# Kernel optimization log

Hardware: AMD Instinct MI355X
Metric: run time of the kernel (lower is better)

## Reference

```python
import jax, jax.numpy as jnp
import numpy as np

E, T, D, N_RBF, N_SBF = 262144, 1048576, 128, 6, 42


def setup_inputs() -> dict:
    key = jax.random.key(0)
    ks = jax.random.split(key, 24)
    s = 0.05
    inp = {
        "m_ji": jax.random.normal(ks[0], (E, D), jnp.float32),
        "e_rbf": jax.random.normal(ks[1], (E, N_RBF), jnp.float32),
        "a_sbf": jax.random.normal(ks[2], (T, N_SBF), jnp.float32),
        "nbr_list": jax.random.randint(ks[3], (E, 2), 0, 65536),
        "kj_idx": jax.random.randint(ks[4], (T,), 0, E),
        "ji_idx": jax.random.randint(ks[5], (T,), 0, E),
        # edge branch params
        "We": jax.random.normal(ks[6], (N_RBF, D), jnp.float32) * s,
        "W_e1": jax.random.normal(ks[7], (D, D), jnp.float32) * s,
        "b_e1": jnp.zeros((D,), jnp.float32),
        "W_e2": jax.random.normal(ks[8], (D, D), jnp.float32) * s,
        "b_e2": jnp.zeros((D,), jnp.float32),
        "W_e3": jax.random.normal(ks[9], (D, D), jnp.float32) * s,
        "b_e3": jnp.zeros((D,), jnp.float32),
        "W_e4": jax.random.normal(ks[10], (D, D), jnp.float32) * s,
        # angle branch params
        "Wa": jax.random.normal(ks[11], (N_SBF, D), jnp.float32) * s,
        "W_a1": jax.random.normal(ks[12], (D, D), jnp.float32) * s,
        "b_a1": jnp.zeros((D,), jnp.float32),
        "W_a2": jax.random.normal(ks[13], (D, D), jnp.float32) * s,
        "b_a2": jnp.zeros((D,), jnp.float32),
        "W_a3": jax.random.normal(ks[14], (D, D), jnp.float32) * s,
        "b_a3": jnp.zeros((D,), jnp.float32),
        "W_a4": jax.random.normal(ks[15], (D, D), jnp.float32) * s,
    }
    return inp


def _mlp(x, W1, b1, W2, b2, W3, b3, W4):
    x = jax.nn.silu(x @ W1 + b1)
    x = jax.nn.silu(x @ W2 + b2)
    x = jax.nn.silu(x @ W3 + b3)
    return x @ W4


def reference(m_ji, e_rbf, a_sbf, nbr_list, kj_idx, ji_idx,
              We, W_e1, b_e1, W_e2, b_e2, W_e3, b_e3, W_e4,
              Wa, W_a1, b_a1, W_a2, b_a2, W_a3, b_a3, W_a4):
    # edge branch: project rbf to embed dim, gate by edge messages  [E, D]
    edge_feats = _mlp((e_rbf @ We) * m_ji, W_e1, b_e1, W_e2, b_e2, W_e3, b_e3, W_e4)
    # angle branch: project sbf, gate by triplet-gathered message sum  [T, D]
    angle_gate = m_ji[kj_idx] + m_ji[ji_idx]
    angle_feats = _mlp((a_sbf @ Wa) * angle_gate, W_a1, b_a1, W_a2, b_a2, W_a3, b_a3, W_a4)
    return (edge_feats, angle_feats)
```

## Files before the change

### kernel.cpp

```cpp
#include <hip/hip_runtime.h>
#include <stdint.h>

typedef __attribute__((ext_vector_type(8))) short bf16x8;
typedef __attribute__((ext_vector_type(4))) float f32x4;
typedef __attribute__((ext_vector_type(8))) unsigned short us8;

static __device__ __forceinline__ unsigned short f2bf_u(float f) {
  __bf16 h = (__bf16)f;
  return __builtin_bit_cast(unsigned short, h);
}
static __device__ __forceinline__ uint32_t pack2bf(float a, float b) {
  return (uint32_t)f2bf_u(a) | ((uint32_t)f2bf_u(b) << 16);
}
static __device__ __forceinline__ float silu_f(float v) {
  float e = __builtin_amdgcn_exp2f(v * -1.44269504088896341f);
  return v * __builtin_amdgcn_rcpf(1.0f + e);
}

template<bool LAST>
static __device__ __forceinline__ void xlayer(
    const char* __restrict__ src, char* __restrict__ dst,
    const bf16x8* wf, const float* __restrict__ bias,
    float* __restrict__ gout, int l15, int q, int w, int rs)
{
  f32x4 bv;
  if (!LAST) bv = *(const f32x4*)(bias + w * 16 + q * 4);
  #pragma unroll
  for (int rg = 0; rg < 8; ++rg) {
    const int row = rg * 16 + l15;
    f32x4 acc = {0.f, 0.f, 0.f, 0.f};
    #pragma unroll
    for (int ks = 0; ks < 4; ++ks) {
      bf16x8 xf = *(const bf16x8*)(src + ((row * 256 + ks * 64 + q * 16) ^ rs));
      acc = __builtin_amdgcn_mfma_f32_16x16x32_bf16(wf[ks], xf, acc, 0, 0, 0);
    }
    if (!LAST) {
      float v0 = silu_f(acc[0] + bv[0]);
      float v1 = silu_f(acc[1] + bv[1]);
      float v2 = silu_f(acc[2] + bv[2]);
      float v3 = silu_f(acc[3] + bv[3]);
      uint2 u; u.x = pack2bf(v0, v1); u.y = pack2bf(v2, v3);
      *(uint2*)(dst + ((row * 256 + w * 32 + q * 8) ^ rs)) = u;
    } else {
      __builtin_nontemporal_store(acc,
          (f32x4*)(gout + (size_t)row * 128 + w * 16 + q * 4));
    }
  }
}

__global__ __launch_bounds__(512)
__attribute__((amdgpu_waves_per_eu(4, 4)))
void angle_kernel(
    const float* __restrict__ m_ji, const float* __restrict__ a_sbf,
    const int* __restrict__ kj, const int* __restrict__ ji,
    const float* __restrict__ b1, const float* __restrict__ b2,
    const float* __restrict__ b3,
    const char* __restrict__ wt4, const char* __restrict__ waT,
    float* __restrict__ out)
{
  extern __shared__ char lds[];
  char* xbA = lds;
  char* xbB = lds + 32768;
  char* aux = lds + 65536;
  const int tid = threadIdx.x, lane = tid & 63, w = tid >> 6;
  const int l15 = lane & 15, q = lane >> 4;
  const int rs = (l15 & 7) << 4;
  const size_t tb = (size_t)blockIdx.x * 128;

  bf16x8 wa0 = *(const bf16x8*)(waT + (w * 2 + 0) * 1024 + lane * 16);
  bf16x8 wa1 = *(const bf16x8*)(waT + (w * 2 + 1) * 1024 + lane * 16);

  int ikj[8], iji[8];
  #pragma unroll
  for (int g = 0; g < 8; ++g) {
    ikj[g] = kj[tb + g * 16 + l15];
    iji[g] = ji[tb + g * 16 + l15];
  }

  f32x4 pk[8], pj[8];
  #pragma unroll
  for (int g = 0; g < 8; ++g) {
    pk[g] = *(const f32x4*)(m_ji + (size_t)ikj[g] * 128 + w * 16 + q * 4);
    pj[g] = *(const f32x4*)(m_ji + (size_t)iji[g] * 128 + w * 16 + q * 4);
  }
  __builtin_amdgcn_sched_barrier(0);

  {
    const float* src = a_sbf + tb * 42;
    #pragma unroll
    for (int j2 = 0; j2 < 8; ++j2) {
      const int i = tid + j2 * 512;
      const int row = i >> 5, p = i & 31;
      const float* rp = src + row * 42 + p * 2;
      float v0 = (p * 2 < 42) ? __builtin_nontemporal_load(rp) : 0.f;
      float v1 = (p * 2 + 1 < 42) ? __builtin_nontemporal_load(rp + 1) : 0.f;
      *(uint32_t*)(aux + ((row * 128 + p * 4) ^ ((row & 7) << 4))) = pack2bf(v0, v1);
    }
  }
  __syncthreads();

  #pragma unroll
  for (int rg = 0; rg < 8; ++rg) {
    const int row = rg * 16 + l15;
    bf16x8 x0f = *(const bf16x8*)(aux + ((row * 128 + q * 16) ^ rs));
    bf16x8 x1f = *(const bf16x8*)(aux + ((row * 128 + 64 + q * 16) ^ rs));
    f32x4 acc = {0.f, 0.f, 0.f, 0.f};
    acc = __builtin_amdgcn_mfma_f32_16x16x32_bf16(wa0, x0f, acc, 0, 0, 0);
    acc = __builtin_amdgcn_mfma_f32_16x16x32_bf16(wa1, x1f, acc, 0, 0, 0);
    f32x4 g = pk[rg] + pj[rg];
    uint2 u;
    u.x = pack2bf(acc[0] * g[0], acc[1] * g[1]);
    u.y = pack2bf(acc[2] * g[2], acc[3] * g[3]);
    *(uint2*)(xbA + ((row * 256 + w * 32 + q * 8) ^ rs)) = u;
  }
  __builtin_amdgcn_sched_barrier(0);

  bf16x8 wfl[4][4];
  #pragma unroll
  for (int L = 0; L < 4; ++L)
    #pragma unroll
    for (int ks = 0; ks < 4; ++ks)
      wfl[L][ks] = *(const bf16x8*)(wt4 + L * 32768 + (w * 4 + ks) * 1024 + lane * 16);

  __syncthreads();

  xlayer<false>(xbA, xbB, wfl[0], b1, nullptr, l15, q, w, rs);
  __syncthreads();
  xlayer<false>(xbB, xbA, wfl[1], b2, nullptr, l15, q, w, rs);
  __syncthreads();
  xlayer<false>(xbA, xbB, wfl[2], b3, nullptr, l15, q, w, rs);
  __syncthreads();
  xlayer<true>(xbB, nullptr, wfl[3], nullptr, out + tb * 128, l15, q, w, rs);
}

__global__ __launch_bounds__(512)
__attribute__((amdgpu_waves_per_eu(4, 4)))
void edge_kernel(
    const float* __restrict__ m_ji, const float* __restrict__ e_rbf,
    const float* __restrict__ b1, const float* __restrict__ b2,
    const float* __restrict__ b3,
    const char* __restrict__ wt4, const char* __restrict__ weT,
    float* __restrict__ out)
{
  extern __shared__ char lds[];
  char* xbA = lds;
  char* xbB = lds + 32768;
  float* auxF = (float*)(lds + 65536);
  const int tid = threadIdx.x, lane = tid & 63, w = tid >> 6;
  const int l15 = lane & 15, q = lane >> 4;
  const int rs = (l15 & 7) << 4;
  const size_t tb = (size_t)blockIdx.x * 128;

  bf16x8 we = *(const bf16x8*)(weT + w * 1024 + lane * 16);

  f32x4 mr[8];
  #pragma unroll
  for (int g = 0; g < 8; ++g)
    mr[g] = *(const f32x4*)(m_ji + (tb + g * 16 + l15) * 128 + w * 16 + q * 4);
  __builtin_amdgcn_sched_barrier(0);

  {
    const float* src = e_rbf + tb * 6;
    auxF[tid] = __builtin_nontemporal_load(src + tid);
    const int i2 = tid + 512;
    if (i2 < 768) auxF[i2] = __builtin_nontemporal_load(src + i2);
  }
  __syncthreads();

  #pragma unroll
  for (int rg = 0; rg < 8; ++rg) {
    const int row = rg * 16 + l15;
    bf16x8 ef;
    #pragma unroll
    for (int j = 0; j < 8; ++j) {
      float v = (j < 6) ? auxF[row * 6 + j] : 0.f;
      unsigned short h = (q == 0 && j < 6) ? f2bf_u(v) : (unsigned short)0;
      ef[j] = (short)h;
    }
    f32x4 acc = {0.f, 0.f, 0.f, 0.f};
    acc = __builtin_amdgcn_mfma_f32_16x16x32_bf16(we, ef, acc, 0, 0, 0);
    f32x4 g = mr[rg];
    uint2 u;
    u.x = pack2bf(acc[0] * g[0], acc[1] * g[1]);
    u.y = pack2bf(acc[2] * g[2], acc[3] * g[3]);
    *(uint2*)(xbA + ((row * 256 + w * 32 + q * 8) ^ rs)) = u;
  }
  __builtin_amdgcn_sched_barrier(0);

  bf16x8 wfl[4][4];
  #pragma unroll
  for (int L = 0; L < 4; ++L)
    #pragma unroll
    for (int ks = 0; ks < 4; ++ks)
      wfl[L][ks] = *(const bf16x8*)(wt4 + L * 32768 + (w * 4 + ks) * 1024 + lane * 16);

  __syncthreads();

  xlayer<false>(xbA, xbB, wfl[0], b1, nullptr, l15, q, w, rs);
  __syncthreads();
  xlayer<false>(xbB, xbA, wfl[1], b2, nullptr, l15, q, w, rs);
  __syncthreads();
  xlayer<false>(xbA, xbB, wfl[2], b3, nullptr, l15, q, w, rs);
  __syncthreads();
  xlayer<true>(xbB, nullptr, wfl[3], nullptr, out + tb * 128, l15, q, w, rs);
}

__global__ void prep_kernel(
    const float* __restrict__ W0, const float* __restrict__ W1,
    const float* __restrict__ W2, const float* __restrict__ W3,
    const float* __restrict__ W4, const float* __restrict__ W5,
    const float* __restrict__ W6, const float* __restrict__ W7,
    const float* __restrict__ Wa, const float* __restrict__ We,
    char* __restrict__ ws)
{
  const int gid = blockIdx.x * 256 + threadIdx.x;
  const int lane = gid & 63;
  const int l15 = lane & 15, q = lane >> 4;
  if (gid < 16384) {
    const int mat = gid >> 11;
    const int ctks = (gid & 2047) >> 6;
    const int n = (ctks >> 2) * 16 + l15;
    const int k0 = (ctks & 3) * 32 + q * 8;
    const float* W;
    switch (mat) {
      case 0: W = W0; break; case 1: W = W1; break;
      case 2: W = W2; break; case 3: W = W3; break;
      case 4: W = W4; break; case 5: W = W5; break;
      case 6: W = W6; break; default: W = W7; break;
    }
    us8 v;
    #pragma unroll
    for (int j = 0; j < 8; ++j) v[j] = f2bf_u(W[(size_t)(k0 + j) * 128 + n]);
    *(us8*)(ws + mat * 32768 + ctks * 1024 + lane * 16) = v;
  } else if (gid < 17408) {
    const int g = gid - 16384;
    const int ctks = g >> 6;
    const int n = (ctks >> 1) * 16 + l15;
    const int k0 = (ctks & 1) * 32 + q * 8;
    us8 v;
    #pragma unroll
    for (int j = 0; j < 8; ++j) {
      const int k = k0 + j;
      v[j] = (k < 42) ? f2bf_u(Wa[(size_t)k * 128 + n]) : (unsigned short)0;
    }
    *(us8*)(ws + 262144 + ctks * 1024 + lane * 16) = v;
  } else if (gid < 17920) {
    const int g = gid - 17408;
    const int ct = g >> 6;
    const int n = ct * 16 + l15;
    const int k0 = q * 8;
    us8 v;
    #pragma unroll
    for (int j = 0; j < 8; ++j) {
      const int k = k0 + j;
      v[j] = (k < 6) ? f2bf_u(We[(size_t)k * 128 + n]) : (unsigned short)0;
    }
    *(us8*)(ws + 278528 + ct * 1024 + lane * 16) = v;
  }
}

extern "C" void kernel_launch(void* const* d_in, const int* in_sizes, int n_in,
                              void* d_out, int out_size, void* d_ws, size_t ws_size,
                              hipStream_t stream) {
  (void)in_sizes; (void)n_in; (void)out_size; (void)ws_size;
  const float* m_ji  = (const float*)d_in[0];
  const float* e_rbf = (const float*)d_in[1];
  const float* a_sbf = (const float*)d_in[2];
  const int*   kj    = (const int*)d_in[4];
  const int*   ji    = (const int*)d_in[5];
  const float* We    = (const float*)d_in[6];
  const float* We1   = (const float*)d_in[7];
  const float* be1   = (const float*)d_in[8];
  const float* We2   = (const float*)d_in[9];
  const float* be2   = (const float*)d_in[10];
  const float* We3   = (const float*)d_in[11];
  const float* be3   = (const float*)d_in[12];
  const float* We4   = (const float*)d_in[13];
  const float* Wa    = (const float*)d_in[14];
  const float* Wa1   = (const float*)d_in[15];
  const float* ba1   = (const float*)d_in[16];
  const float* Wa2   = (const float*)d_in[17];
  const float* ba2   = (const float*)d_in[18];
  const float* Wa3   = (const float*)d_in[19];
  const float* ba3   = (const float*)d_in[20];
  const float* Wa4   = (const float*)d_in[21];
  char* ws = (char*)d_ws;
  float* out = (float*)d_out;

  hipFuncSetAttribute((const void*)edge_kernel,
                      hipFuncAttributeMaxDynamicSharedMemorySize, 68608);
  hipFuncSetAttribute((const void*)angle_kernel,
                      hipFuncAttributeMaxDynamicSharedMemorySize, 81920);

  prep_kernel<<<70, 256, 0, stream>>>(
      We1, We2, We3, We4, Wa1, Wa2, Wa3, Wa4, Wa, We, ws);
  edge_kernel<<<262144 / 128, 512, 68608, stream>>>(
      m_ji, e_rbf, be1, be2, be3, ws, ws + 278528, out);
  angle_kernel<<<1048576 / 128, 512, 81920, stream>>>(
      m_ji, a_sbf, kj, ji, ba1, ba2, ba3, ws + 131072, ws + 262144,
      out + (size_t)262144 * 128);
}
```

Measured before the change: 615.7 us.

## Shrink MLP blocks to 32 rows with two waves and stream weights per layer

Both the edge and angle kernels now use 128-thread blocks that each handle 32 rows. Each wave computes four 16-column tiles across two row groups. The input projections load a_sbf and e_rbf rows straight from global memory into MFMA fragments, dropping the LDS staging pass. LDS use falls to 16 KB per block, and layer weights are reloaded from global or cache inside each layer instead of being held in registers. The aim is higher occupancy and less per-block setup and synchronisation, at the cost of several times more weight traffic through the caches per row processed.

```diff
diff --git a/kernel.cpp b/kernel.cpp
--- a/kernel.cpp
+++ b/kernel.cpp
@@ -4,52 +4,81 @@
 typedef __attribute__((ext_vector_type(8))) short bf16x8;
 typedef __attribute__((ext_vector_type(4))) float f32x4;
 typedef __attribute__((ext_vector_type(8))) unsigned short us8;
+typedef __bf16 bf16v2 __attribute__((ext_vector_type(2)));
+
+#define T_CNT 1048576
+#define E_CNT 262144
 
 static __device__ __forceinline__ unsigned short f2bf_u(float f) {
   __bf16 h = (__bf16)f;
   return __builtin_bit_cast(unsigned short, h);
 }
 static __device__ __forceinline__ uint32_t pack2bf(float a, float b) {
-  return (uint32_t)f2bf_u(a) | ((uint32_t)f2bf_u(b) << 16);
+  bf16v2 t; t[0] = (__bf16)a; t[1] = (__bf16)b;
+  return __builtin_bit_cast(uint32_t, t);
 }
 static __device__ __forceinline__ float silu_f(float v) {
   float e = __builtin_amdgcn_exp2f(v * -1.44269504088896341f);
   return v * __builtin_amdgcn_rcpf(1.0f + e);
 }
+static __device__ __forceinline__ bf16x8 frag8(f32x4 a, f32x4 b) {
+  union { bf16x8 v; uint32_t u[4]; } r;
+  r.u[0] = pack2bf(a[0], a[1]); r.u[1] = pack2bf(a[2], a[3]);
+  r.u[2] = pack2bf(b[0], b[1]); r.u[3] = pack2bf(b[2], b[3]);
+  return r.v;
+}
 
 template<bool LAST>
-static __device__ __forceinline__ void xlayer(
+static __device__ __forceinline__ void layer_mfma(
     const char* __restrict__ src, char* __restrict__ dst,
-    const bf16x8* wf, const float* __restrict__ bias,
-    float* __restrict__ gout, int l15, int q, int w, int rs)
-{
-  f32x4 bv;
-  if (!LAST) bv = *(const f32x4*)(bias + w * 16 + q * 4);
-  #pragma unroll
-  for (int rg = 0; rg < 8; ++rg) {
+    const char* __restrict__ wbase,
+    const float* __restrict__ bias,
+    float* __restrict__ gout,
+    int l15, int q, int w, int rs)
+{
+  f32x4 acc[2][4];
+  #pragma unroll
+  for (int rg = 0; rg < 2; ++rg)
+    #pragma unroll
+    for (int c = 0; c < 4; ++c) { f32x4 z = {0.f,0.f,0.f,0.f}; acc[rg][c] = z; }
+
+  const int lane16 = (l15 | (q << 4)) * 16;
+  #pragma unroll
+  for (int ks = 0; ks < 4; ++ks) {
+    bf16x8 wf[4];
+    #pragma unroll
+    for (int c = 0; c < 4; ++c)
+      wf[c] = *(const bf16x8*)(wbase + (((w * 4 + c) * 4 + ks) << 10) + lane16);
+    bf16x8 xf0 = *(const bf16x8*)(src + ((l15 * 256 + ks * 64 + q * 16) ^ rs));
+    bf16x8 xf1 = *(const bf16x8*)(src + (((16 + l15) * 256 + ks * 64 + q * 16) ^ rs));
+    #pragma unroll
+    for (int c = 0; c < 4; ++c) {
+      acc[0][c] = __builtin_amdgcn_mfma_f32_16x16x32_bf16(wf[c], xf0, acc[0][c], 0, 0, 0);
+      acc[1][c] = __builtin_amdgcn_mfma_f32_16x16x32_bf16(wf[c], xf1, acc[1][c], 0, 0, 0);
+    }
+  }
+
+  #pragma unroll
+  for (int rg = 0; rg < 2; ++rg) {
     const int row = rg * 16 + l15;
-    f32x4 acc = {0.f, 0.f, 0.f, 0.f};
-    #pragma unroll
-    for (int ks = 0; ks < 4; ++ks) {
-      bf16x8 xf = *(const bf16x8*)(src + ((row * 256 + ks * 64 + q * 16) ^ rs));
-      acc = __builtin_amdgcn_mfma_f32_16x16x32_bf16(wf[ks], xf, acc, 0, 0, 0);
-    }
-    if (!LAST) {
-      float v0 = silu_f(acc[0] + bv[0]);
-      float v1 = silu_f(acc[1] + bv[1]);
-      float v2 = silu_f(acc[2] + bv[2]);
-      float v3 = silu_f(acc[3] + bv[3]);
-      uint2 u; u.x = pack2bf(v0, v1); u.y = pack2bf(v2, v3);
-      *(uint2*)(dst + ((row * 256 + w * 32 + q * 8) ^ rs)) = u;
-    } else {
-      __builtin_nontemporal_store(acc,
-          (f32x4*)(gout + (size_t)row * 128 + w * 16 + q * 4));
-    }
-  }
-}
-
-__global__ __launch_bounds__(512)
-__attribute__((amdgpu_waves_per_eu(4, 4)))
+    #pragma unroll
+    for (int c = 0; c < 4; ++c) {
+      if (!LAST) {
+        f32x4 bv = *(const f32x4*)(bias + w * 64 + c * 16 + q * 4);
+        uint2 u;
+        u.x = pack2bf(silu_f(acc[rg][c][0] + bv[0]), silu_f(acc[rg][c][1] + bv[1]));
+        u.y = pack2bf(silu_f(acc[rg][c][2] + bv[2]), silu_f(acc[rg][c][3] + bv[3]));
+        *(uint2*)(dst + ((row * 256 + w * 128 + c * 32 + q * 8) ^ rs)) = u;
+      } else {
+        __builtin_nontemporal_store(acc[rg][c],
+            (f32x4*)(gout + (size_t)row * 128 + w * 64 + c * 16 + q * 4));
+      }
+    }
+  }
+}
+
+__global__ __launch_bounds__(128)
+__attribute__((amdgpu_waves_per_eu(4, 5)))
 void angle_kernel(
     const float* __restrict__ m_ji, const float* __restrict__ a_sbf,
     const int* __restrict__ kj, const int* __restrict__ ji,
@@ -58,83 +87,60 @@
     const char* __restrict__ wt4, const char* __restrict__ waT,
     float* __restrict__ out)
 {
-  extern __shared__ char lds[];
-  char* xbA = lds;
-  char* xbB = lds + 32768;
-  char* aux = lds + 65536;
+  __shared__ __align__(16) char xbA[8192];
+  __shared__ __align__(16) char xbB[8192];
   const int tid = threadIdx.x, lane = tid & 63, w = tid >> 6;
   const int l15 = lane & 15, q = lane >> 4;
   const int rs = (l15 & 7) << 4;
-  const size_t tb = (size_t)blockIdx.x * 128;
-
-  bf16x8 wa0 = *(const bf16x8*)(waT + (w * 2 + 0) * 1024 + lane * 16);
-  bf16x8 wa1 = *(const bf16x8*)(waT + (w * 2 + 1) * 1024 + lane * 16);
-
-  int ikj[8], iji[8];
-  #pragma unroll
-  for (int g = 0; g < 8; ++g) {
-    ikj[g] = kj[tb + g * 16 + l15];
-    iji[g] = ji[tb + g * 16 + l15];
-  }
-
-  f32x4 pk[8], pj[8];
-  #pragma unroll
-  for (int g = 0; g < 8; ++g) {
-    pk[g] = *(const f32x4*)(m_ji + (size_t)ikj[g] * 128 + w * 16 + q * 4);
-    pj[g] = *(const f32x4*)(m_ji + (size_t)iji[g] * 128 + w * 16 + q * 4);
-  }
-  __builtin_amdgcn_sched_barrier(0);
-
-  {
-    const float* src = a_sbf + tb * 42;
-    #pragma unroll
-    for (int j2 = 0; j2 < 8; ++j2) {
-      const int i = tid + j2 * 512;
-      const int row = i >> 5, p = i & 31;
-      const float* rp = src + row * 42 + p * 2;
-      float v0 = (p * 2 < 42) ? __builtin_nontemporal_load(rp) : 0.f;
-      float v1 = (p * 2 + 1 < 42) ? __builtin_nontemporal_load(rp + 1) : 0.f;
-      *(uint32_t*)(aux + ((row * 128 + p * 4) ^ ((row & 7) << 4))) = pack2bf(v0, v1);
-    }
-  }
-  __syncthreads();
-
-  #pragma unroll
-  for (int rg = 0; rg < 8; ++rg) {
+  const size_t tb = (size_t)blockIdx.x * 32;
+  const int lane16 = lane * 16;
+
+  #pragma unroll
+  for (int rg = 0; rg < 2; ++rg) {
     const int row = rg * 16 + l15;
-    bf16x8 x0f = *(const bf16x8*)(aux + ((row * 128 + q * 16) ^ rs));
-    bf16x8 x1f = *(const bf16x8*)(aux + ((row * 128 + 64 + q * 16) ^ rs));
-    f32x4 acc = {0.f, 0.f, 0.f, 0.f};
-    acc = __builtin_amdgcn_mfma_f32_16x16x32_bf16(wa0, x0f, acc, 0, 0, 0);
-    acc = __builtin_amdgcn_mfma_f32_16x16x32_bf16(wa1, x1f, acc, 0, 0, 0);
-    f32x4 g = pk[rg] + pj[rg];
-    uint2 u;
-    u.x = pack2bf(acc[0] * g[0], acc[1] * g[1]);
-    u.y = pack2bf(acc[2] * g[2], acc[3] * g[3]);
-    *(uint2*)(xbA + ((row * 256 + w * 32 + q * 8) ^ rs)) = u;
-  }
-  __builtin_amdgcn_sched_barrier(0);
-
-  bf16x8 wfl[4][4];
-  #pragma unroll
-  for (int L = 0; L < 4; ++L)
-    #pragma unroll
-    for (int ks = 0; ks < 4; ++ks)
-      wfl[L][ks] = *(const bf16x8*)(wt4 + L * 32768 + (w * 4 + ks) * 1024 + lane * 16);
-
-  __syncthreads();
-
-  xlayer<false>(xbA, xbB, wfl[0], b1, nullptr, l15, q, w, rs);
-  __syncthreads();
-  xlayer<false>(xbB, xbA, wfl[1], b2, nullptr, l15, q, w, rs);
-  __syncthreads();
-  xlayer<false>(xbA, xbB, wfl[2], b3, nullptr, l15, q, w, rs);
-  __syncthreads();
-  xlayer<true>(xbB, nullptr, wfl[3], nullptr, out + tb * 128, l15, q, w, rs);
-}
-
-__global__ __launch_bounds__(512)
-__attribute__((amdgpu_waves_per_eu(4, 4)))
+    const size_t grow = tb + row;
+    const int ikj = kj[grow], iji = ji[grow];
+    const float* ap = a_sbf + grow * 42;
+    f32x4 a0 = *(const f32x4*)(ap + q * 8);
+    f32x4 a1 = *(const f32x4*)(ap + q * 8 + 4);
+    f32x4 c0 = {0.f,0.f,0.f,0.f}, c1 = {0.f,0.f,0.f,0.f};
+    if (q == 0) { c0 = *(const f32x4*)(ap + 32); c1 = *(const f32x4*)(ap + 36); }
+    else if (q == 1) { float2 t = *(const float2*)(ap + 40); c0[0] = t.x; c0[1] = t.y; }
+    bf16x8 f0 = frag8(a0, a1);
+    bf16x8 f1 = frag8(c0, c1);
+    #pragma unroll
+    for (int c = 0; c < 4; ++c) {
+      const int ct = w * 4 + c;
+      bf16x8 wa0 = *(const bf16x8*)(waT + ((ct * 2 + 0) << 10) + lane16);
+      bf16x8 wa1 = *(const bf16x8*)(waT + ((ct * 2 + 1) << 10) + lane16);
+      f32x4 acc = {0.f,0.f,0.f,0.f};
+      acc = __builtin_amdgcn_mfma_f32_16x16x32_bf16(wa0, f0, acc, 0, 0, 0);
+      acc = __builtin_amdgcn_mfma_f32_16x16x32_bf16(wa1, f1, acc, 0, 0, 0);
+      const float* bk = m_ji + (size_t)ikj * 128 + ct * 16 + q * 4;
+      const float* bj = m_ji + (size_t)iji * 128 + ct * 16 + q * 4;
+      f32x4 pk = *(const f32x4*)(bk);
+      f32x4 pj = *(const f32x4*)(bj);
+      f32x4 g = pk + pj;
+      uint2 u;
+      u.x = pack2bf(acc[0] * g[0], acc[1] * g[1]);
+      u.y = pack2bf(acc[2] * g[2], acc[3] * g[3]);
+      *(uint2*)(xbA + ((row * 256 + w * 128 + c * 32 + q * 8) ^ rs)) = u;
+    }
+  }
+  __syncthreads();
+
+  layer_mfma<false>(xbA, xbB, wt4,           b1, nullptr, l15, q, w, rs);
+  __syncthreads();
+  layer_mfma<false>(xbB, xbA, wt4 + 32768,   b2, nullptr, l15, q, w, rs);
+  __syncthreads();
+  layer_mfma<false>(xbA, xbB, wt4 + 65536,   b3, nullptr, l15, q, w, rs);
+  __syncthreads();
+  layer_mfma<true >(xbB, nullptr, wt4 + 98304, nullptr,
+                    out + tb * 128, l15, q, w, rs);
+}
+
+__global__ __launch_bounds__(128)
+__attribute__((amdgpu_waves_per_eu(4, 5)))
 void edge_kernel(
     const float* __restrict__ m_ji, const float* __restrict__ e_rbf,
     const float* __restrict__ b1, const float* __restrict__ b2,
@@ -142,67 +148,49 @@
     const char* __restrict__ wt4, const char* __restrict__ weT,
     float* __restrict__ out)
 {
-  extern __shared__ char lds[];
-  char* xbA = lds;
-  char* xbB = lds + 32768;
-  float* auxF = (float*)(lds + 65536);
+  __shared__ __align__(16) char xbA[8192];
+  __shared__ __align__(16) char xbB[8192];
   const int tid = threadIdx.x, lane = tid & 63, w = tid >> 6;
   const int l15 = lane & 15, q = lane >> 4;
   const int rs = (l15 & 7) << 4;
-  const size_t tb = (size_t)blockIdx.x * 128;
-
-  bf16x8 we = *(const bf16x8*)(weT + w * 1024 + lane * 16);
-
-  f32x4 mr[8];
-  #pragma unroll
-  for (int g = 0; g < 8; ++g)
-    mr[g] = *(const f32x4*)(m_ji + (tb + g * 16 + l15) * 128 + w * 16 + q * 4);
-  __builtin_amdgcn_sched_barrier(0);
-
-  {
-    const float* src = e_rbf + tb * 6;
-    auxF[tid] = __builtin_nontemporal_load(src + tid);
-    const int i2 = tid + 512;
-    if (i2 < 768) auxF[i2] = __builtin_nontemporal_load(src + i2);
-  }
-  __syncthreads();
-
-  #pragma unroll
-  for (int rg = 0; rg < 8; ++rg) {
+  const size_t tb = (size_t)blockIdx.x * 32;
+  const int lane16 = lane * 16;
+
+  #pragma unroll
+  for (int rg = 0; rg < 2; ++rg) {
     const int row = rg * 16 + l15;
-    bf16x8 ef;
-    #pragma unroll
-    for (int j = 0; j < 8; ++j) {
-      float v = (j < 6) ? auxF[row * 6 + j] : 0.f;
-      unsigned short h = (q == 0 && j < 6) ? f2bf_u(v) : (unsigned short)0;
-      ef[j] = (short)h;
-    }
-    f32x4 acc = {0.f, 0.f, 0.f, 0.f};
-    acc = __builtin_amdgcn_mfma_f32_16x16x32_bf16(we, ef, acc, 0, 0, 0);
-    f32x4 g = mr[rg];
-    uint2 u;
-    u.x = pack2bf(acc[0] * g[0], acc[1] * g[1]);
-    u.y = pack2bf(acc[2] * g[2], acc[3] * g[3]);
-    *(uint2*)(xbA + ((row * 256 + w * 32 + q * 8) ^ rs)) = u;
-  }
-  __builtin_amdgcn_sched_barrier(0);
-
-  bf16x8 wfl[4][4];
-  #pragma unroll
-  for (int L = 0; L < 4; ++L)
-    #pragma unroll
-    for (int ks = 0; ks < 4; ++ks)
-      wfl[L][ks] = *(const bf16x8*)(wt4 + L * 32768 + (w * 4 + ks) * 1024 + lane * 16);
-
-  __syncthreads();
-
-  xlayer<false>(xbA, xbB, wfl[0], b1, nullptr, l15, q, w, rs);
-  __syncthreads();
-  xlayer<false>(xbB, xbA, wfl[1], b2, nullptr, l15, q, w, rs);
-  __syncthreads();
-  xlayer<false>(xbA, xbB, wfl[2], b3, nullptr, l15, q, w, rs);
-  __syncthreads();
-  xlayer<true>(xbB, nullptr, wfl[3], nullptr, out + tb * 128, l15, q, w, rs);
+    const size_t grow = tb + row;
+    const float* ep = e_rbf + grow * 6;
+    f32x4 a0 = {0.f,0.f,0.f,0.f}, a1 = {0.f,0.f,0.f,0.f};
+    if (q == 0) {
+      a0 = *(const f32x4*)(ep);
+      float2 t = *(const float2*)(ep + 4);
+      a1[0] = t.x; a1[1] = t.y;
+    }
+    bf16x8 ef = frag8(a0, a1);
+    #pragma unroll
+    for (int c = 0; c < 4; ++c) {
+      const int ct = w * 4 + c;
+      bf16x8 we = *(const bf16x8*)(weT + (ct << 10) + lane16);
+      f32x4 acc = {0.f,0.f,0.f,0.f};
+      acc = __builtin_amdgcn_mfma_f32_16x16x32_bf16(we, ef, acc, 0, 0, 0);
+      f32x4 g = *(const f32x4*)(m_ji + grow * 128 + ct * 16 + q * 4);
+      uint2 u;
+      u.x = pack2bf(acc[0] * g[0], acc[1] * g[1]);
+      u.y = pack2bf(acc[2] * g[2], acc[3] * g[3]);
+      *(uint2*)(xbA + ((row * 256 + w * 128 + c * 32 + q * 8) ^ rs)) = u;
+    }
+  }
+  __syncthreads();
+
+  layer_mfma<false>(xbA, xbB, wt4,           b1, nullptr, l15, q, w, rs);
+  __syncthreads();
+  layer_mfma<false>(xbB, xbA, wt4 + 32768,   b2, nullptr, l15, q, w, rs);
+  __syncthreads();
+  layer_mfma<false>(xbA, xbB, wt4 + 65536,   b3, nullptr, l15, q, w, rs);
+  __syncthreads();
+  layer_mfma<true >(xbB, nullptr, wt4 + 98304, nullptr,
+                    out + tb * 128, l15, q, w, rs);
 }
 
 __global__ void prep_kernel(
@@ -287,16 +275,11 @@
   char* ws = (char*)d_ws;
   float* out = (float*)d_out;
 
-  hipFuncSetAttribute((const void*)edge_kernel,
-                      hipFuncAttributeMaxDynamicSharedMemorySize, 68608);
-  hipFuncSetAttribute((const void*)angle_kernel,
-                      hipFuncAttributeMaxDynamicSharedMemorySize, 81920);
-
   prep_kernel<<<70, 256, 0, stream>>>(
       We1, We2, We3, We4, Wa1, Wa2, Wa3, Wa4, Wa, We, ws);
-  edge_kernel<<<262144 / 128, 512, 68608, stream>>>(
+  edge_kernel<<<E_CNT / 32, 128, 0, stream>>>(
       m_ji, e_rbf, be1, be2, be3, ws, ws + 278528, out);
-  angle_kernel<<<1048576 / 128, 512, 81920, stream>>>(
+  angle_kernel<<<T_CNT / 32, 128, 0, stream>>>(
       m_ji, a_sbf, kj, ji, ba1, ba2, ba3, ws + 131072, ws + 262144,
-      out + (size_t)262144 * 128);
-}
+      out + (size_t)E_CNT * 128);
+}
```

Result: faster. 580.0 us (-5.8%).
